# Kernel tuning notes

Measured on AMD Instinct MI355X. Metric: run time of the kernel, lower is better.

Reference implementation:

```python
import jax, jax.numpy as jnp
import numpy as np

N = 50000
E = 1600000
F_IN = 503
F_H = 128
NEG_SLOPE = 0.2


def setup_inputs() -> dict:
    key = jax.random.key(0)
    ks = jax.random.split(key, 24)
    s = 0.05
    inp = {
        "x": jax.random.normal(ks[0], (N, F_IN), jnp.float32),
        "edge_index": jax.random.randint(ks[1], (2, E), 0, N, jnp.int64),
        "edge_attr": jax.random.uniform(ks[2], (E, 1), jnp.float32),
        "input_mask": jax.random.uniform(ks[3], (N, 1), jnp.float32),
        # GATConv layer 1 (in=503, out=128, heads=1, edge_dim=1)
        "W1": jax.random.normal(ks[4], (F_IN, F_H), jnp.float32) * s,
        "b1": jnp.zeros((F_H,), jnp.float32),
        "as1": jax.random.normal(ks[5], (F_H,), jnp.float32) * s,
        "ad1": jax.random.normal(ks[6], (F_H,), jnp.float32) * s,
        "We1": jax.random.normal(ks[7], (1, F_H), jnp.float32) * s,
        "ae1": jax.random.normal(ks[8], (F_H,), jnp.float32) * s,
        # GATConv layer 2 (in=128, out=128)
        "W2": jax.random.normal(ks[9], (F_H, F_H), jnp.float32) * s,
        "b2": jnp.zeros((F_H,), jnp.float32),
        "as2": jax.random.normal(ks[10], (F_H,), jnp.float32) * s,
        "ad2": jax.random.normal(ks[11], (F_H,), jnp.float32) * s,
        "We2": jax.random.normal(ks[12], (1, F_H), jnp.float32) * s,
        "ae2": jax.random.normal(ks[13], (F_H,), jnp.float32) * s,
        # edge/node heads
        "Wb": jax.random.normal(ks[14], (F_H, 1), jnp.float32) * s,
        "bb": jnp.zeros((1,), jnp.float32),
        "Ww": jax.random.normal(ks[15], (F_H, 1), jnp.float32) * s,
        "bw": jnp.zeros((1,), jnp.float32),
    }
    return inp


def _gat_conv(x, src, dst, ea, W, b, a_src_vec, a_dst_vec, We, a_edge_vec):
    """PyG GATConv, heads=1, add_self_loops=True, fill_value='mean'."""
    n = x.shape[0]
    loop = jnp.arange(n)
    # self-loop edge attrs = mean of incoming edge attrs (0 if none)
    deg = jax.ops.segment_sum(jnp.ones(dst.shape, ea.dtype), dst, num_segments=n)
    ea_loop = jax.ops.segment_sum(ea, dst, num_segments=n) / jnp.maximum(deg, 1.0)[:, None]
    s = jnp.concatenate([src, loop])
    d = jnp.concatenate([dst, loop])
    ea2 = jnp.concatenate([ea, ea_loop], axis=0)  # [E+N, 1]

    h = x @ W                              # [N, F_H]
    a_s = h @ a_src_vec                    # [N]
    a_d = h @ a_dst_vec                    # [N]
    a_e = (ea2 @ We) @ a_edge_vec          # [E+N]

    alpha = jax.nn.leaky_relu(a_s[s] + a_d[d] + a_e, NEG_SLOPE)
    # scatter-softmax over destination neighborhoods (every node has a self loop)
    m = jax.lax.stop_gradient(jax.ops.segment_max(alpha, d, num_segments=n))
    ex = jnp.exp(alpha - m[d])
    den = jax.ops.segment_sum(ex, d, num_segments=n)
    coef = ex / den[d]                     # [E+N]

    out = jax.ops.segment_sum(coef[:, None] * h[s], d, num_segments=n)
    return out + b


def reference(x, edge_index, edge_attr, input_mask,
              W1, b1, as1, ad1, We1, ae1,
              W2, b2, as2, ad2, We2, ae2,
              Wb, bb, Ww, bw):
    src, dst = edge_index[0], edge_index[1]
    h = jax.nn.relu(_gat_conv(x, src, dst, edge_attr, W1, b1, as1, ad1, We1, ae1))
    h = jax.nn.relu(_gat_conv(h, src, dst, edge_attr, W2, b2, as2, ad2, We2, ae2))
    b_out = (h @ Wb + bb) * input_mask          # [N, 1]
    # directed graph: is_directed() is True, so use all edges
    w = ((h[src] + h[dst]) * 0.5) @ Ww + bw     # [E, 1]
    return (w, b_out)
```

## Files before the change

kernel.cpp:

```cpp
#include <hip/hip_runtime.h>
#include <hip/hip_fp16.h>

#define FH 128
#define NEG_SLOPE 0.2f
#define GBM 64
#define GBK 64
#define HT 1024
#define TB 8
#define NWMAX 12512


typedef _Float16 f16x8 __attribute__((ext_vector_type(8)));
typedef float f32x4 __attribute__((ext_vector_type(4)));

__global__ __launch_bounds__(HT) void hist_kernel(const int* __restrict__ ei,
                                                  unsigned short* __restrict__ hist,
                                                  int E, int N) {
  __shared__ unsigned int lh[NWMAX];
  const int b = blockIdx.x, tid = threadIdx.x;
  const int nw = (N + 3) >> 2;
  for (int j = tid; j < nw; j += HT) lh[j] = 0u;
  __syncthreads();
  const int i0 = b * (HT * TB) + tid * TB;
  if (i0 + TB <= E) {
    int4 da = *(const int4*)&ei[E + i0];
    int4 db = *(const int4*)&ei[E + i0 + 4];
    int dv[8] = {da.x, da.y, da.z, da.w, db.x, db.y, db.z, db.w};
    #pragma unroll
    for (int k = 0; k < 8; k++)
      atomicAdd(&lh[dv[k] >> 2], 1u << ((dv[k] & 3) * 8));
  } else {
    for (int i = i0; i < E; i++) {
      int d = ei[E + i];
      atomicAdd(&lh[d >> 2], 1u << ((d & 3) * 8));
    }
  }
  __syncthreads();
  unsigned short* hb = hist + (size_t)b * N;
  for (int j = tid; j < nw; j += HT) {
    unsigned v = lh[j];
    int bin = j * 4;
    if (bin + 3 < N) {
      ushort4 o;
      o.x = v & 255u; o.y = (v >> 8) & 255u; o.z = (v >> 16) & 255u; o.w = v >> 24;
      *(ushort4*)&hb[bin] = o;
    } else {
      for (int k = 0; k < 4 && bin + k < N; k++) hb[bin + k] = (v >> (k * 8)) & 255u;
    }
  }
}

__global__ void colscan_kernel(unsigned short* __restrict__ hist,
                               int* __restrict__ cnt, int N, int NBr) {
  int bin = blockIdx.x * 256 + threadIdx.x;
  if (bin >= N) return;
  int s = 0, b = 0;
  for (; b + 8 <= NBr; b += 8) {
    int t[8];
    #pragma unroll
    for (int k = 0; k < 8; k++) t[k] = hist[(size_t)(b + k) * N + bin];
    #pragma unroll
    for (int k = 0; k < 8; k++) {
      hist[(size_t)(b + k) * N + bin] = (unsigned short)s;
      s += t[k];
    }
  }
  for (; b < NBr; b++) {
    int t = hist[(size_t)b * N + bin];
    hist[(size_t)b * N + bin] = (unsigned short)s;
    s += t;
  }
  cnt[bin] = s;
}

__global__ void scan_blocksum(const int* __restrict__ deg, int* __restrict__ bsum, int n) {
  __shared__ int sm[256];
  int i = blockIdx.x * 256 + threadIdx.x;
  sm[threadIdx.x] = (i < n) ? deg[i] : 0;
  __syncthreads();
  for (int off = 128; off > 0; off >>= 1) {
    if (threadIdx.x < off) sm[threadIdx.x] += sm[threadIdx.x + off];
    __syncthreads();
  }
  if (threadIdx.x == 0) bsum[blockIdx.x] = sm[0];
}

__global__ void scan_bsum(int* __restrict__ bsum, int nb, int* __restrict__ rowptr, int N) {
  __shared__ int sm[1024];
  int t = threadIdx.x;
  int v = (t < nb) ? bsum[t] : 0;
  sm[t] = v;
  __syncthreads();
  for (int off = 1; off < 1024; off <<= 1) {
    int u = (t >= off) ? sm[t - off] : 0;
    __syncthreads();
    sm[t] += u;
    __syncthreads();
  }
  if (t < nb) bsum[t] = sm[t] - v;
  if (t == 1023) rowptr[N] = sm[1023];
}

__global__ void scan_final(const int* __restrict__ deg, const int* __restrict__ bsum,
                           int* __restrict__ rowptr, int n) {
  __shared__ int sm[256];
  int i = blockIdx.x * 256 + threadIdx.x;
  int v = (i < n) ? deg[i] : 0;
  sm[threadIdx.x] = v;
  __syncthreads();
  for (int off = 1; off < 256; off <<= 1) {
    int u = (threadIdx.x >= off) ? sm[threadIdx.x - off] : 0;
    __syncthreads();
    sm[threadIdx.x] += u;
    __syncthreads();
  }
  if (i < n) rowptr[i] = bsum[blockIdx.x] + sm[threadIdx.x] - v;
}

__global__ __launch_bounds__(HT) void place_kernel(const int* __restrict__ ei,
                                                   const float* __restrict__ ea,
                                                   const int* __restrict__ rowptr,
                                                   const unsigned short* __restrict__ off,
                                                   unsigned int* __restrict__ pack,
                                                   int E, int N) {
  __shared__ unsigned int lc[NWMAX];
  const int b = blockIdx.x, tid = threadIdx.x;
  const int nw = (N + 3) >> 2;
  for (int j = tid; j < nw; j += HT) lc[j] = 0u;
  __syncthreads();
  const unsigned short* __restrict__ ob = off + (size_t)b * N;
  const int i0 = b * (HT * TB) + tid * TB;
  if (i0 + TB <= E) {
    int4 sa = *(const int4*)&ei[i0];
    int4 sb = *(const int4*)&ei[i0 + 4];
    int4 da = *(const int4*)&ei[E + i0];
    int4 db = *(const int4*)&ei[E + i0 + 4];
    float4 aa = *(const float4*)&ea[i0];
    float4 ab = *(const float4*)&ea[i0 + 4];
    int sv[8] = {sa.x, sa.y, sa.z, sa.w, sb.x, sb.y, sb.z, sb.w};
    int dv[8] = {da.x, da.y, da.z, da.w, db.x, db.y, db.z, db.w};
    float av[8] = {aa.x, aa.y, aa.z, aa.w, ab.x, ab.y, ab.z, ab.w};
    unsigned rr[8];
    #pragma unroll
    for (int k = 0; k < 8; k++)
      rr[k] = atomicAdd(&lc[dv[k] >> 2], 1u << ((dv[k] & 3) * 8));
    int pos[8];
    #pragma unroll
    for (int k = 0; k < 8; k++)
      pos[k] = rowptr[dv[k]] + (int)ob[dv[k]] + (int)((rr[k] >> ((dv[k] & 3) * 8)) & 255u);
    #pragma unroll
    for (int k = 0; k < 8; k++)
      pack[pos[k]] = ((unsigned)sv[k] << 16) | __half_as_ushort(__float2half(av[k]));
  } else {
    for (int i = i0; i < E; i++) {
      int d = ei[E + i];
      unsigned r = atomicAdd(&lc[d >> 2], 1u << ((d & 3) * 8));
      int local = (r >> ((d & 3) * 8)) & 255;
      int pos = rowptr[d] + (int)ob[d] + local;
      pack[pos] = ((unsigned)ei[i] << 16) | __half_as_ushort(__float2half(ea[i]));
    }
  }
}

__global__ void cvec_kernel(const float* __restrict__ We1, const float* __restrict__ ae1,
                            const float* __restrict__ We2, const float* __restrict__ ae2,
                            float* __restrict__ cv) {
  int l = threadIdx.x;
  float s1 = We1[l] * ae1[l] + We1[l + 64] * ae1[l + 64];
  float s2 = We2[l] * ae2[l] + We2[l + 64] * ae2[l + 64];
  for (int off = 32; off; off >>= 1) { s1 += __shfl_down(s1, off); s2 += __shfl_down(s2, off); }
  if (l == 0) { cv[0] = s1; cv[1] = s2; }
}

__global__ void wcvt_kernel(const float* __restrict__ W, __half* __restrict__ Wt,
                            int K, int Kpad, int perm) {
  int idx = blockIdx.x * 256 + threadIdx.x;
  if (idx >= 128 * Kpad) return;
  int n = idx / Kpad, p = idx - n * Kpad;
  int k = perm ? ((p & 7) * 16 + (p >> 3)) : p;
  Wt[idx] = (k < K) ? __float2half(W[(size_t)k * 128 + n]) : __float2half(0.f);
}

__global__ __launch_bounds__(256, 4) void mfma_gemm_kernel(
    const float* __restrict__ X, const __half* __restrict__ Wt_,
    const float* __restrict__ avs, const float* __restrict__ avd,
    __half* __restrict__ H16, float* __restrict__ a_s, float* __restrict__ a_d,
    int M, int K, int Kpad) {
  __shared__ _Float16 Bl[2 * 8 * 64 * 8];
  const _Float16* __restrict__ Wt = (const _Float16*)Wt_;
  const int tid  = threadIdx.x;
  const int lane = tid & 63;
  const int w    = tid >> 6;
  const int m0   = blockIdx.x * GBM;

  f32x4 acc[8];
  #pragma unroll
  for (int i = 0; i < 8; i++) acc[i] = (f32x4){0.f, 0.f, 0.f, 0.f};

  const int arow   = m0 + w * 16 + (lane & 15);
  const int arow_c = arow < M ? arow : (M - 1);
  const float* __restrict__ Xrow = X + (size_t)arow_c * K;
  const int kgrp = (lane >> 4) * 8;

  const int sg = tid & 7, snb = tid >> 3;

  for (int k0 = 0; k0 < Kpad; k0 += GBK) {
    #pragma unroll
    for (int i = 0; i < 4; i++) {
      int n = snb + 32 * i;
      f16x8 v = *(const f16x8*)(Wt + (size_t)n * Kpad + k0 + sg * 8);
      int kt = sg >> 2, nt = n >> 4;
      int fl = (n & 15) + (sg & 3) * 16;
      *(f16x8*)&Bl[((kt * 8 + nt) * 64 + fl) * 8] = v;
    }
    __syncthreads();
    const bool fast = (k0 + GBK <= K);
    #pragma unroll
    for (int kt = 0; kt < 2; kt++) {
      int kb = k0 + kt * 32 + kgrp;
      f16x8 af;
      if (fast) {
        #pragma unroll
        for (int j = 0; j < 8; j++) af[j] = (_Float16)Xrow[kb + j];
      } else {
        #pragma unroll
        for (int j = 0; j < 8; j++)
          af[j] = (kb + j < K) ? (_Float16)Xrow[kb + j] : (_Float16)0.f;
      }
      #pragma unroll
      for (int nt = 0; nt < 8; nt++) {
        f16x8 bf = *(const f16x8*)&Bl[((kt * 8 + nt) * 64 + lane) * 8];
        acc[nt] = __builtin_amdgcn_mfma_f32_16x16x32_f16(af, bf, acc[nt], 0, 0, 0);
      }
    }
    __syncthreads();
  }

  const int rbase = m0 + w * 16 + (lane >> 4) * 4;
  const int col   = lane & 15;
  float as_v[8], ad_v[8];
  #pragma unroll
  for (int nt = 0; nt < 8; nt++) {
    as_v[nt] = avs[nt * 16 + col];
    ad_v[nt] = avd[nt * 16 + col];
  }
  #pragma unroll
  for (int r = 0; r < 4; r++) {
    int gm = rbase + r;
    float ps = 0.f, pd = 0.f;
    #pragma unroll
    for (int nt = 0; nt < 8; nt++) {
      ps += acc[nt][r] * as_v[nt];
      pd += acc[nt][r] * ad_v[nt];
    }
    #pragma unroll
    for (int msk = 1; msk < 16; msk <<= 1) {
      ps += __shfl_xor(ps, msk);
      pd += __shfl_xor(pd, msk);
    }
    if (gm < M) {
      __half2 h0 = __floats2half2_rn(acc[0][r], acc[1][r]);
      __half2 h1 = __floats2half2_rn(acc[2][r], acc[3][r]);
      __half2 h2 = __floats2half2_rn(acc[4][r], acc[5][r]);
      __half2 h3 = __floats2half2_rn(acc[6][r], acc[7][r]);
      uint4 u;
      u.x = *(unsigned*)&h0; u.y = *(unsigned*)&h1;
      u.z = *(unsigned*)&h2; u.w = *(unsigned*)&h3;
      *(uint4*)&H16[(size_t)gm * FH + col * 8] = u;
      if (col == 0) { a_s[gm] = ps; a_d[gm] = pd; }
    }
  }
}

__global__ __launch_bounds__(256) void agg_kernel(
    const __half* __restrict__ H16, const int* __restrict__ rowptr,
    const unsigned int* __restrict__ pack,
    const float* __restrict__ a_s, const float* __restrict__ a_d,
    const float* __restrict__ cv, int cidx,
    const float* __restrict__ bias,
    float* __restrict__ Hout, int N) {
  const int node = (blockIdx.x * 256 + threadIdx.x) >> 6;
  const int lane = threadIdx.x & 63;
  const int slot = lane >> 4, sl = lane & 15;
  if (node >= N) return;
  const _Float16* __restrict__ Hh = (const _Float16*)H16;
  const float c   = cv[cidx];
  const float adn = a_d[node];
  const int beg = rowptr[node], end = rowptr[node + 1];

  float acc[8] = {0.f, 0.f, 0.f, 0.f, 0.f, 0.f, 0.f, 0.f};
  float den = 0.f, ea_tot = 0.f;

  for (int p = beg + slot; p < end; p += 4) {
    unsigned w0 = pack[p];
    int s0 = w0 >> 16;
    float e0 = __half2float(__ushort_as_half((unsigned short)(w0 & 0xffff)));
    float al = a_s[s0] + adn + c * e0;
    al = fmaxf(al, NEG_SLOPE * al);
    float ex = __expf(al);
    f16x8 h = *(const f16x8*)(Hh + (size_t)s0 * FH + sl * 8);
    ea_tot += e0;
    den += ex;
    #pragma unroll
    for (int j = 0; j < 8; j++) acc[j] += ex * (float)h[j];
  }
  ea_tot += __shfl_xor(ea_tot, 16); ea_tot += __shfl_xor(ea_tot, 32);
  den    += __shfl_xor(den,    16); den    += __shfl_xor(den,    32);
  #pragma unroll
  for (int j = 0; j < 8; j++) {
    acc[j] += __shfl_xor(acc[j], 16);
    acc[j] += __shfl_xor(acc[j], 32);
  }
  {
    int dg = end - beg;
    float eal = ea_tot / fmaxf((float)dg, 1.f);
    float al = a_s[node] + adn + c * eal;
    al = fmaxf(al, NEG_SLOPE * al);
    float ex = __expf(al);
    f16x8 h = *(const f16x8*)(Hh + (size_t)node * FH + sl * 8);
    den += ex;
    #pragma unroll
    for (int j = 0; j < 8; j++) acc[j] += ex * (float)h[j];
  }
  if (slot == 0) {
    float inv = 1.f / den;
    float bi[8];
    #pragma unroll
    for (int j = 0; j < 8; j++) bi[j] = bias[j * 16 + sl];
    float4 o0, o1;
    o0.x = fmaxf(acc[0] * inv + bi[0], 0.f);
    o0.y = fmaxf(acc[1] * inv + bi[1], 0.f);
    o0.z = fmaxf(acc[2] * inv + bi[2], 0.f);
    o0.w = fmaxf(acc[3] * inv + bi[3], 0.f);
    o1.x = fmaxf(acc[4] * inv + bi[4], 0.f);
    o1.y = fmaxf(acc[5] * inv + bi[5], 0.f);
    o1.z = fmaxf(acc[6] * inv + bi[6], 0.f);
    o1.w = fmaxf(acc[7] * inv + bi[7], 0.f);
    *(float4*)&Hout[(size_t)node * FH + sl * 8]     = o0;
    *(float4*)&Hout[(size_t)node * FH + sl * 8 + 4] = o1;
  }
}

__global__ void node_head_kernel(const float* __restrict__ H, const float* __restrict__ Wb,
                                 const float* __restrict__ bb, const float* __restrict__ Ww,
                                 const float* __restrict__ mask,
                                 float* __restrict__ bout, float* __restrict__ p, int N) {
  int gid = blockIdx.x * 256 + threadIdx.x;
  int node = gid >> 6, lane = threadIdx.x & 63;
  if (node >= N) return;
  int p0 = lane * 2, p1 = p0 + 1;
  int f0 = ((p0 & 7) << 4) + (p0 >> 3);
  int f1 = ((p1 & 7) << 4) + (p1 >> 3);
  float2 h = *(const float2*)&H[(size_t)node * FH + p0];
  float sb = h.x * Wb[f0] + h.y * Wb[f1];
  float sw = h.x * Ww[f0] + h.y * Ww[f1];
  for (int off = 32; off; off >>= 1) { sb += __shfl_down(sb, off); sw += __shfl_down(sw, off); }
  if (lane == 0) {
    bout[node] = (sb + bb[0]) * mask[node];
    p[node]    = sw;
  }
}

__global__ void edge_head_kernel(const int* __restrict__ ei, const float* __restrict__ p,
                                 const float* __restrict__ bw, float* __restrict__ w, int E) {
  int base = (blockIdx.x * 256 + threadIdx.x) * 4;
  if (base >= E) return;
  float b = bw[0];
  if (base + 4 <= E) {
    int4 s = *(const int4*)&ei[base];
    int4 d = *(const int4*)&ei[E + base];
    float4 o;
    o.x = 0.5f * (p[s.x] + p[d.x]) + b;
    o.y = 0.5f * (p[s.y] + p[d.y]) + b;
    o.z = 0.5f * (p[s.z] + p[d.z]) + b;
    o.w = 0.5f * (p[s.w] + p[d.w]) + b;
    *(float4*)&w[base] = o;
  } else {
    for (int e = base; e < E; e++)
      w[e] = 0.5f * (p[ei[e]] + p[ei[E + e]]) + b;
  }
}

extern "C" void kernel_launch(void* const* d_in, const int* in_sizes, int n_in,
                              void* d_out, int out_size, void* d_ws, size_t ws_size,
                              hipStream_t stream) {
  (void)n_in; (void)out_size; (void)ws_size;
  const float* x    = (const float*)d_in[0];
  const int*   ei   = (const int*)  d_in[1];
  const float* ea   = (const float*)d_in[2];
  const float* mask = (const float*)d_in[3];
  const float* W1   = (const float*)d_in[4];
  const float* b1   = (const float*)d_in[5];
  const float* as1  = (const float*)d_in[6];
  const float* ad1  = (const float*)d_in[7];
  const float* We1  = (const float*)d_in[8];
  const float* ae1  = (const float*)d_in[9];
  const float* W2   = (const float*)d_in[10];
  const float* b2   = (const float*)d_in[11];
  const float* as2  = (const float*)d_in[12];
  const float* ad2  = (const float*)d_in[13];
  const float* We2  = (const float*)d_in[14];
  const float* ae2  = (const float*)d_in[15];
  const float* Wb   = (const float*)d_in[16];
  const float* bb   = (const float*)d_in[17];
  const float* Ww   = (const float*)d_in[18];
  const float* bw   = (const float*)d_in[19];

  const int N  = in_sizes[3];
  const int E  = in_sizes[1] / 2;
  const int K1 = in_sizes[0] / N;
  const int K1p = (K1 + GBK - 1) & ~(GBK - 1);
  const int NBr = (E + HT * TB - 1) / (HT * TB);

  char* ws = (char*)d_ws;
  size_t off0 = 0;
  auto alloc = [&](size_t bytes) -> char* {
    char* q = ws + off0;
    off0 = (off0 + bytes + 255) & ~(size_t)255;
    return q;
  };
  int*   cnt    = (int*)  alloc((size_t)N * 4);
  int*   rowptr = (int*)  alloc((size_t)(N + 1) * 4);
  int*   bsum   = (int*)  alloc(1024 * 4);
  unsigned short* hist = (unsigned short*)alloc((size_t)NBr * N * 2);
  unsigned int*   pack = (unsigned int*)  alloc((size_t)E * 4);
  float* a_s    = (float*)alloc((size_t)N * 4);
  float* a_d    = (float*)alloc((size_t)N * 4);
  __half* H16   = (__half*)alloc((size_t)N * FH * 2);
  float* HB     = (float*)alloc((size_t)N * FH * 4);
  float* pbuf   = (float*)alloc((size_t)N * 4);
  float* cv     = (float*)alloc(8);
  __half* W1t   = (__half*)alloc((size_t)FH * K1p * 2);
  __half* W2t   = (__half*)alloc((size_t)FH * FH * 2);

  float* w_out = (float*)d_out;
  float* b_out = (float*)d_out + E;

  const int nb  = (N + 255) / 256;
  const int gb  = (N + GBM - 1) / GBM;
  const int wbk = ((size_t)N * 64 + 255) / 256;
  const int ab  = (N + 3) / 4;
  const int eb4 = (E + 1023) / 1024;

  hist_kernel   <<<NBr, HT, 0, stream>>>(ei, hist, E, N);
  colscan_kernel<<<nb, 256, 0, stream>>>(hist, cnt, N, NBr);
  scan_blocksum <<<nb, 256, 0, stream>>>(cnt, bsum, N);
  scan_bsum     <<<1, 1024, 0, stream>>>(bsum, nb, rowptr, N);
  scan_final    <<<nb, 256, 0, stream>>>(cnt, bsum, rowptr, N);
  place_kernel  <<<NBr, HT, 0, stream>>>(ei, ea, rowptr, hist, pack, E, N);
  cvec_kernel   <<<1, 64, 0, stream>>>(We1, ae1, We2, ae2, cv);
  wcvt_kernel   <<<(128 * K1p + 255) / 256, 256, 0, stream>>>(W1, W1t, K1, K1p, 0);
  wcvt_kernel   <<<(128 * FH + 255) / 256, 256, 0, stream>>>(W2, W2t, FH, FH, 1);

  mfma_gemm_kernel<<<gb, 256, 0, stream>>>(x, W1t, as1, ad1, H16, a_s, a_d, N, K1, K1p);
  agg_kernel  <<<ab, 256, 0, stream>>>(H16, rowptr, pack, a_s, a_d, cv, 0, b1, HB, N);
  mfma_gemm_kernel<<<gb, 256, 0, stream>>>(HB, W2t, as2, ad2, H16, a_s, a_d, N, FH, FH);
  agg_kernel  <<<ab, 256, 0, stream>>>(H16, rowptr, pack, a_s, a_d, cv, 1, b2, HB, N);
  node_head_kernel<<<wbk, 256, 0, stream>>>(HB, Wb, bb, Ww, mask, b_out, pbuf, N);
  edge_head_kernel<<<eb4, 256, 0, stream>>>(ei, pbuf, bw, w_out, E);
}
```

Measured before the change: 276.0 us.

## Pre-pack GEMM A operand into fp16 MFMA tile layout and unroll aggregation

Adds an xpack kernel that converts x to fp16 in a tiled layout matching the MFMA A-fragment order. The GEMM can then load each fragment with one vector load instead of eight strided fp32 loads with conversion. Layer-1 aggregation now writes its output directly in this packed fp16 layout for the second GEMM, and the packed buffer shares memory with the histogram scratch. The aggregation loop is unrolled by two with separate accumulators to expose more memory-level parallelism. The cost is an extra pass over x, and the tiling assumes N is a multiple of 16.

Result: slower. 315.0 us (+14.1%).

```diff
diff --git a/kernel.cpp b/kernel.cpp
--- a/kernel.cpp
+++ b/kernel.cpp
@@ -181,26 +181,50 @@
   Wt[idx] = (k < K) ? __float2half(W[(size_t)k * 128 + n]) : __float2half(0.f);
 }
 
+__global__ __launch_bounds__(256) void xpack_kernel(const float* __restrict__ X,
+                                                    __half* __restrict__ A16,
+                                                    int M, int K, int Kpad) {
+  __shared__ _Float16 T[64 * 16 * 8];
+  const int mg = blockIdx.x, tid = threadIdx.x;
+  const int nq = Kpad >> 3;
+  const int r = tid >> 4, qs = tid & 15;
+  const float* __restrict__ Xr = X + (size_t)(mg * 16 + r) * K;
+  for (int q = qs; q < nq; q += 16) {
+    f16x8 v;
+    int kb = q * 8;
+    #pragma unroll
+    for (int j = 0; j < 8; j++)
+      v[j] = (kb + j < K) ? (_Float16)Xr[kb + j] : (_Float16)0.f;
+    *(f16x8*)&T[(q * 16 + r) * 8] = v;
+  }
+  __syncthreads();
+  const int total = nq * 128;
+  _Float16* dst = (_Float16*)A16 + (size_t)mg * total;
+  for (int o = tid * 8; o < total; o += 256 * 8)
+    *(f16x8*)&dst[o] = *(const f16x8*)&T[o];
+}
+
 __global__ __launch_bounds__(256, 4) void mfma_gemm_kernel(
-    const float* __restrict__ X, const __half* __restrict__ Wt_,
+    const __half* __restrict__ A16_, const __half* __restrict__ Wt_,
     const float* __restrict__ avs, const float* __restrict__ avd,
     __half* __restrict__ H16, float* __restrict__ a_s, float* __restrict__ a_d,
-    int M, int K, int Kpad) {
+    int M, int Kpad) {
   __shared__ _Float16 Bl[2 * 8 * 64 * 8];
-  const _Float16* __restrict__ Wt = (const _Float16*)Wt_;
+  const _Float16* __restrict__ A16 = (const _Float16*)A16_;
+  const _Float16* __restrict__ Wt  = (const _Float16*)Wt_;
   const int tid  = threadIdx.x;
   const int lane = tid & 63;
   const int w    = tid >> 6;
   const int m0   = blockIdx.x * GBM;
+  const int nq   = Kpad >> 3;
 
   f32x4 acc[8];
   #pragma unroll
   for (int i = 0; i < 8; i++) acc[i] = (f32x4){0.f, 0.f, 0.f, 0.f};
 
-  const int arow   = m0 + w * 16 + (lane & 15);
-  const int arow_c = arow < M ? arow : (M - 1);
-  const float* __restrict__ Xrow = X + (size_t)arow_c * K;
-  const int kgrp = (lane >> 4) * 8;
+  const int mgc = min(m0 / 16 + w, M / 16 - 1);
+  const _Float16* __restrict__ Abase =
+      A16 + (size_t)mgc * nq * 128 + (lane >> 4) * 128 + (lane & 15) * 8;
 
   const int sg = tid & 7, snb = tid >> 3;
 
@@ -214,19 +238,9 @@
       *(f16x8*)&Bl[((kt * 8 + nt) * 64 + fl) * 8] = v;
     }
     __syncthreads();
-    const bool fast = (k0 + GBK <= K);
     #pragma unroll
     for (int kt = 0; kt < 2; kt++) {
-      int kb = k0 + kt * 32 + kgrp;
-      f16x8 af;
-      if (fast) {
-        #pragma unroll
-        for (int j = 0; j < 8; j++) af[j] = (_Float16)Xrow[kb + j];
-      } else {
-        #pragma unroll
-        for (int j = 0; j < 8; j++)
-          af[j] = (kb + j < K) ? (_Float16)Xrow[kb + j] : (_Float16)0.f;
-      }
+      f16x8 af = *(const f16x8*)(Abase + (size_t)k0 * 16 + kt * 512);
       #pragma unroll
       for (int nt = 0; nt < 8; nt++) {
         f16x8 bf = *(const f16x8*)&Bl[((kt * 8 + nt) * 64 + lane) * 8];
@@ -272,13 +286,14 @@
   }
 }
 
+template<int OUTP>
 __global__ __launch_bounds__(256) void agg_kernel(
     const __half* __restrict__ H16, const int* __restrict__ rowptr,
     const unsigned int* __restrict__ pack,
     const float* __restrict__ a_s, const float* __restrict__ a_d,
     const float* __restrict__ cv, int cidx,
     const float* __restrict__ bias,
-    float* __restrict__ Hout, int N) {
+    float* __restrict__ HoutF, __half* __restrict__ HoutP, int N) {
   const int node = (blockIdx.x * 256 + threadIdx.x) >> 6;
   const int lane = threadIdx.x & 63;
   const int slot = lane >> 4, sl = lane & 15;
@@ -289,9 +304,32 @@
   const int beg = rowptr[node], end = rowptr[node + 1];
 
   float acc[8] = {0.f, 0.f, 0.f, 0.f, 0.f, 0.f, 0.f, 0.f};
-  float den = 0.f, ea_tot = 0.f;
-
-  for (int p = beg + slot; p < end; p += 4) {
+  float accB[8] = {0.f, 0.f, 0.f, 0.f, 0.f, 0.f, 0.f, 0.f};
+  float den = 0.f, ea_tot = 0.f, denB = 0.f, eaB = 0.f;
+
+  int p = beg + slot;
+  for (; p + 4 < end; p += 8) {
+    unsigned w0 = pack[p], w1 = pack[p + 4];
+    int s0 = w0 >> 16, s1 = w1 >> 16;
+    float e0 = __half2float(__ushort_as_half((unsigned short)(w0 & 0xffff)));
+    float e1 = __half2float(__ushort_as_half((unsigned short)(w1 & 0xffff)));
+    float as0 = a_s[s0], as1 = a_s[s1];
+    f16x8 h0 = *(const f16x8*)(Hh + (size_t)s0 * FH + sl * 8);
+    f16x8 h1 = *(const f16x8*)(Hh + (size_t)s1 * FH + sl * 8);
+    float al0 = as0 + adn + c * e0;
+    float al1 = as1 + adn + c * e1;
+    al0 = fmaxf(al0, NEG_SLOPE * al0);
+    al1 = fmaxf(al1, NEG_SLOPE * al1);
+    float ex0 = __expf(al0), ex1 = __expf(al1);
+    ea_tot += e0; eaB += e1;
+    den += ex0; denB += ex1;
+    #pragma unroll
+    for (int j = 0; j < 8; j++) {
+      acc[j]  += ex0 * (float)h0[j];
+      accB[j] += ex1 * (float)h1[j];
+    }
+  }
+  for (; p < end; p += 4) {
     unsigned w0 = pack[p];
     int s0 = w0 >> 16;
     float e0 = __half2float(__ushort_as_half((unsigned short)(w0 & 0xffff)));
@@ -304,6 +342,9 @@
     #pragma unroll
     for (int j = 0; j < 8; j++) acc[j] += ex * (float)h[j];
   }
+  den += denB; ea_tot += eaB;
+  #pragma unroll
+  for (int j = 0; j < 8; j++) acc[j] += accB[j];
   ea_tot += __shfl_xor(ea_tot, 16); ea_tot += __shfl_xor(ea_tot, 32);
   den    += __shfl_xor(den,    16); den    += __shfl_xor(den,    32);
   #pragma unroll
@@ -324,20 +365,22 @@
   }
   if (slot == 0) {
     float inv = 1.f / den;
-    float bi[8];
-    #pragma unroll
-    for (int j = 0; j < 8; j++) bi[j] = bias[j * 16 + sl];
-    float4 o0, o1;
-    o0.x = fmaxf(acc[0] * inv + bi[0], 0.f);
-    o0.y = fmaxf(acc[1] * inv + bi[1], 0.f);
-    o0.z = fmaxf(acc[2] * inv + bi[2], 0.f);
-    o0.w = fmaxf(acc[3] * inv + bi[3], 0.f);
-    o1.x = fmaxf(acc[4] * inv + bi[4], 0.f);
-    o1.y = fmaxf(acc[5] * inv + bi[5], 0.f);
-    o1.z = fmaxf(acc[6] * inv + bi[6], 0.f);
-    o1.w = fmaxf(acc[7] * inv + bi[7], 0.f);
-    *(float4*)&Hout[(size_t)node * FH + sl * 8]     = o0;
-    *(float4*)&Hout[(size_t)node * FH + sl * 8 + 4] = o1;
+    float v[8];
+    #pragma unroll
+    for (int j = 0; j < 8; j++)
+      v[j] = fmaxf(acc[j] * inv + bias[j * 16 + sl], 0.f);
+    if (OUTP) {
+      f16x8 o;
+      #pragma unroll
+      for (int j = 0; j < 8; j++) o[j] = (_Float16)v[j];
+      int mg = node >> 4, r = node & 15;
+      *(f16x8*)((_Float16*)HoutP + (((size_t)mg * 16 + sl) * 16 + r) * 8) = o;
+    } else {
+      float4 o0 = make_float4(v[0], v[1], v[2], v[3]);
+      float4 o1 = make_float4(v[4], v[5], v[6], v[7]);
+      *(float4*)&HoutF[(size_t)node * FH + sl * 8]     = o0;
+      *(float4*)&HoutF[(size_t)node * FH + sl * 8 + 4] = o1;
+    }
   }
 }
 
@@ -411,6 +454,7 @@
   const int K1 = in_sizes[0] / N;
   const int K1p = (K1 + GBK - 1) & ~(GBK - 1);
   const int NBr = (E + HT * TB - 1) / (HT * TB);
+  const int NT  = N / 16;
 
   char* ws = (char*)d_ws;
   size_t off0 = 0;
@@ -422,8 +466,13 @@
   int*   cnt    = (int*)  alloc((size_t)N * 4);
   int*   rowptr = (int*)  alloc((size_t)(N + 1) * 4);
   int*   bsum   = (int*)  alloc(1024 * 4);
-  unsigned short* hist = (unsigned short*)alloc((size_t)NBr * N * 2);
-  unsigned int*   pack = (unsigned int*)  alloc((size_t)E * 4);
+  size_t uszA = (size_t)NBr * N * 2;
+  size_t uszB = (size_t)NT * (K1p / 8) * 256;
+  char*  uni  = alloc(uszA > uszB ? uszA : uszB);
+  unsigned short* hist = (unsigned short*)uni;
+  __half* XA16 = (__half*)uni;
+  __half* HB16 = (__half*)uni;
+  unsigned int* pack = (unsigned int*)alloc((size_t)E * 4);
   float* a_s    = (float*)alloc((size_t)N * 4);
   float* a_d    = (float*)alloc((size_t)N * 4);
   __half* H16   = (__half*)alloc((size_t)N * FH * 2);
@@ -451,11 +500,14 @@
   cvec_kernel   <<<1, 64, 0, stream>>>(We1, ae1, We2, ae2, cv);
   wcvt_kernel   <<<(128 * K1p + 255) / 256, 256, 0, stream>>>(W1, W1t, K1, K1p, 0);
   wcvt_kernel   <<<(128 * FH + 255) / 256, 256, 0, stream>>>(W2, W2t, FH, FH, 1);
-
-  mfma_gemm_kernel<<<gb, 256, 0, stream>>>(x, W1t, as1, ad1, H16, a_s, a_d, N, K1, K1p);
-  agg_kernel  <<<ab, 256, 0, stream>>>(H16, rowptr, pack, a_s, a_d, cv, 0, b1, HB, N);
-  mfma_gemm_kernel<<<gb, 256, 0, stream>>>(HB, W2t, as2, ad2, H16, a_s, a_d, N, FH, FH);
-  agg_kernel  <<<ab, 256, 0, stream>>>(H16, rowptr, pack, a_s, a_d, cv, 1, b2, HB, N);
+  xpack_kernel  <<<NT, 256, 0, stream>>>(x, XA16, N, K1, K1p);
+
+  mfma_gemm_kernel<<<gb, 256, 0, stream>>>(XA16, W1t, as1, ad1, H16, a_s, a_d, N, K1p);
+  agg_kernel<1><<<ab, 256, 0, stream>>>(H16, rowptr, pack, a_s, a_d, cv, 0, b1,
+                                        nullptr, HB16, N);
+  mfma_gemm_kernel<<<gb, 256, 0, stream>>>(HB16, W2t, as2, ad2, H16, a_s, a_d, N, FH);
+  agg_kernel<0><<<ab, 256, 0, stream>>>(H16, rowptr, pack, a_s, a_d, cv, 1, b2,
+                                        HB, nullptr, N);
   node_head_kernel<<<wbk, 256, 0, stream>>>(HB, Wb, bb, Ww, mask, b_out, pbuf, N);
   edge_head_kernel<<<eb4, 256, 0, stream>>>(ei, pbuf, bw, w_out, E);
 }
```
